# Performance work log

Hardware: AMD Instinct MI355X
Metric: run time of the kernel (lower is better)

Reference implementation:

```python
import jax, jax.numpy as jnp
import numpy as np

DIM = 128
CODEBOOK_SIZE = 1024


def setup_inputs() -> dict:
    key = jax.random.key(0)
    kx, ke = jax.random.split(key)
    x = jax.random.normal(kx, (16, 4096, DIM), dtype=jnp.float32)
    # kaiming_uniform_ on (codebook_size, dim): bound = sqrt(6 / fan_in), fan_in = dim
    bound = float(np.sqrt(6.0 / DIM))
    embed = jax.random.uniform(ke, (CODEBOOK_SIZE, DIM), dtype=jnp.float32,
                               minval=-bound, maxval=bound)
    return {"x": x, "embed": embed}


def reference(x, embed):
    orig_shape = x.shape
    flat = x.reshape(-1, x.shape[-1])                     # [N, D]
    x2 = jnp.sum(flat * flat, axis=1, keepdims=True)      # [N, 1]
    e2 = jnp.sum(embed * embed, axis=1)                   # [K]
    dist = -(x2 - 2.0 * (flat @ embed.T) + e2[None, :])   # [N, K]
    embed_ind = jnp.argmax(dist, axis=-1)                 # [N]
    embed_ind = embed_ind.reshape(orig_shape[:-1])        # [B, S]
    quantize = jnp.take(embed, embed_ind, axis=0)         # [B, S, D]
    return quantize, embed_ind
```

## Files before the change

### kernel.cpp

```cpp
#include <hip/hip_runtime.h>

#define DIM     128
#define NCODES  1024
#define TILE_M  64
#define LDSS    136
#define DELTA   0.02f
#define RPB     4
#define RGRID   1024

typedef __attribute__((ext_vector_type(8))) _Float16 half8;
typedef __attribute__((ext_vector_type(4))) _Float16 half4;
typedef __attribute__((ext_vector_type(4))) float    f32x4;


__global__ __launch_bounds__(256) void setup_kernel(
    const float* __restrict__ embed, double* __restrict__ e2d,
    float* __restrict__ e2f, _Float16* __restrict__ eh,
    float* __restrict__ embedT, int* __restrict__ cnt)
{
  __shared__ float tile[64][132];
  __shared__ double psum[4][64];
  if (blockIdx.x == 0 && threadIdx.x == 0) *cnt = 0;
  const int c0 = blockIdx.x * 64;
  const int t  = threadIdx.x;

  const f32x4* E4 = (const f32x4*)(embed + (size_t)c0 * DIM);
  #pragma unroll
  for (int i = 0; i < 8; ++i) {
    int e = t + i * 256;
    int r = e >> 5, c4 = e & 31;
    f32x4 v = E4[e];
    *(f32x4*)&tile[r][c4 * 4] = v;
    half4 h;
    h[0] = (_Float16)v[0]; h[1] = (_Float16)v[1];
    h[2] = (_Float16)v[2]; h[3] = (_Float16)v[3];
    *(half4*)&eh[(size_t)(c0 + r) * DIM + c4 * 4] = h;
  }
  __syncthreads();

  {
    int r = t & 63, part = t >> 6;
    double s = 0.0;
    #pragma unroll
    for (int k = 0; k < 32; ++k) {
      float v = tile[r][part * 32 + k];
      s += (double)v * v;
    }
    psum[part][r] = s;
  }
  __syncthreads();
  if (t < 64) {
    double s = psum[0][t] + psum[1][t] + psum[2][t] + psum[3][t];
    e2d[c0 + t] = s;
    e2f[c0 + t] = (float)s;
  }

  #pragma unroll
  for (int i = 0; i < 32; ++i) {
    int idx = t + i * 256;
    int k = idx >> 6, c = idx & 63;
    embedT[(size_t)k * NCODES + c0 + c] = tile[c][k];
  }
}

__global__ __launch_bounds__(256)
__attribute__((amdgpu_waves_per_eu(3)))
void pass1_kernel(
    const float* __restrict__ x, const float* __restrict__ embed,
    const _Float16* __restrict__ eh, const float* __restrict__ e2f,
    float* __restrict__ outQ, float* __restrict__ outIdx,
    int* __restrict__ cnt, int* __restrict__ list)
{
  __shared__ _Float16 xh[TILE_M * LDSS];
  __shared__ float rb_best[4][TILE_M];
  __shared__ float rb_sec [4][TILE_M];
  __shared__ int   fidx[TILE_M];

  const int tid  = threadIdx.x;
  const int row0 = blockIdx.x * TILE_M;

  {
    const f32x4* x4 = (const f32x4*)(x + (size_t)row0 * DIM);
    #pragma unroll
    for (int i = 0; i < 8; ++i) {
      int e = tid + i * 256;
      int r = e >> 5, c4 = e & 31;
      f32x4 v = x4[e];
      half4 h;
      h[0] = (_Float16)v[0]; h[1] = (_Float16)v[1];
      h[2] = (_Float16)v[2]; h[3] = (_Float16)v[3];
      *(half4*)&xh[r * LDSS + c4 * 4] = h;
    }
  }
  __syncthreads();

  const int l  = tid & 63, w = tid >> 6;
  const int rl = l & 15,  q = l >> 4;
  const int col0 = q * 8;

  half8 afrag[4][4];
  #pragma unroll
  for (int m = 0; m < 4; ++m)
    #pragma unroll
    for (int ks = 0; ks < 4; ++ks)
      afrag[m][ks] = *(const half8*)&xh[(m * 16 + rl) * LDSS + ks * 32 + col0];

  float bestp[16], secp[16];
  #pragma unroll
  for (int s = 0; s < 16; ++s) { bestp[s] = 3.0e38f; secp[s] = 3.3e38f; }

  const int codeBase = w * 256;
  const _Float16* ehw = eh + (size_t)(codeBase + rl) * DIM + col0;

  half8 bbuf[2][4];
  float e2buf[2];
  #pragma unroll
  for (int ks = 0; ks < 4; ++ks) bbuf[0][ks] = *(const half8*)(ehw + ks * 32);
  e2buf[0] = e2f[codeBase + rl];

  #pragma unroll 2
  for (int ch = 0; ch < 16; ++ch) {
    const int cur = ch & 1, nxt = cur ^ 1;
    const int mycode = codeBase + ch * 16 + rl;
    if (ch < 15) {
      const _Float16* ehn = ehw + (size_t)(ch + 1) * (16 * DIM);
      #pragma unroll
      for (int ks = 0; ks < 4; ++ks) bbuf[nxt][ks] = *(const half8*)(ehn + ks * 32);
      e2buf[nxt] = e2f[mycode + 16];
    }
    const float e2c = e2buf[cur];

    #pragma unroll
    for (int m = 0; m < 4; ++m) {
      f32x4 acc = (f32x4){0.f, 0.f, 0.f, 0.f};
      #pragma unroll
      for (int ks = 0; ks < 4; ++ks)
        acc = __builtin_amdgcn_mfma_f32_16x16x32_f16(afrag[m][ks], bbuf[cur][ks], acc, 0, 0, 0);
      #pragma unroll
      for (int r = 0; r < 4; ++r) {
        const int s = m * 4 + r;
        float sc  = fmaf(-2.0f, acc[r], e2c);
        float scp = __int_as_float((__float_as_int(sc) & ~1023) | mycode);
        secp[s]  = __builtin_amdgcn_fmed3f(bestp[s], scp, secp[s]);
        bestp[s] = fminf(bestp[s], scp);
      }
    }
  }

  #pragma unroll
  for (int off = 1; off < 16; off <<= 1) {
    #pragma unroll
    for (int s = 0; s < 16; ++s) {
      float ob = __shfl_xor(bestp[s], off, 16);
      float os = __shfl_xor(secp[s],  off, 16);
      secp[s]  = fminf(__builtin_amdgcn_fmed3f(bestp[s], ob, secp[s]), os);
      bestp[s] = fminf(bestp[s], ob);
    }
  }
  if (rl == 0) {
    #pragma unroll
    for (int m = 0; m < 4; ++m)
      #pragma unroll
      for (int r = 0; r < 4; ++r) {
        int s = m * 4 + r;
        int row = m * 16 + q * 4 + r;
        rb_best[w][row] = bestp[s];
        rb_sec [w][row] = secp[s];
      }
  }
  __syncthreads();

  if (tid < TILE_M) {
    float bv = rb_best[0][tid], sv = rb_sec[0][tid];
    #pragma unroll
    for (int ww = 1; ww < 4; ++ww) {
      float ob = rb_best[ww][tid], os = rb_sec[ww][tid];
      sv = fminf(__builtin_amdgcn_fmed3f(bv, ob, sv), os);
      bv = fminf(bv, ob);
    }
    int bi = __float_as_int(bv) & 1023;
    int grow = row0 + tid;
    outIdx[grow] = (float)bi;
    fidx[tid] = bi;
    if (sv - bv <= DELTA + fabsf(bv) * 4.8828125e-4f) {
      int p = atomicAdd(cnt, 1);
      list[p] = grow;
    }
  }
  __syncthreads();

  {
    const f32x4* E4   = (const f32x4*)embed;
    f32x4*       out4 = (f32x4*)(outQ + (size_t)row0 * DIM);
    #pragma unroll
    for (int i = 0; i < 8; ++i) {
      int e = tid + i * 256;
      int r = e >> 5, c4 = e & 31;
      out4[e] = E4[fidx[r] * 32 + c4];
    }
  }
}

__global__ __launch_bounds__(256) void refine2_kernel(
    const float* __restrict__ x, const float* __restrict__ embed,
    const float* __restrict__ embedT,
    const double* __restrict__ e2d, const float* __restrict__ e2f,
    float* __restrict__ outQ, float* __restrict__ outIdx,
    const int* __restrict__ cnt, const int* __restrict__ list)
{
  __shared__ f32x4 xst[DIM];
  __shared__ float rb1[RPB][4], rb2[RPB][4];
  __shared__ int   ri1[RPB][4], ri2[RPB][4];
  __shared__ int   cand[RPB][2];

  const int t = threadIdx.x;
  const int l = t & 63, w = t >> 6;
  const int n = *cnt;
  float* xsf = (float*)xst;

  for (int base = blockIdx.x * RPB; base < n; base += RGRID * RPB) {
    const int nr = min(RPB, n - base);
    #pragma unroll
    for (int i = 0; i < 2; ++i) {
      int idx = t + i * 256;
      int r = idx >> 7, k = idx & 127;
      float v = 0.f;
      if (r < nr) v = x[(size_t)list[base + r] * DIM + k];
      xsf[k * RPB + r] = v;
    }
    __syncthreads();

    f32x4 dot[RPB];
    #pragma unroll
    for (int r = 0; r < RPB; ++r) dot[r] = (f32x4){0.f, 0.f, 0.f, 0.f};
    const f32x4* eT4 = (const f32x4*)embedT;
    #pragma unroll 4
    for (int k = 0; k < DIM; ++k) {
      f32x4 e4  = eT4[k * 256 + t];
      f32x4 xk4 = xst[k];
      #pragma unroll
      for (int r = 0; r < RPB; ++r) {
        dot[r][0] = fmaf(xk4[r], e4[0], dot[r][0]);
        dot[r][1] = fmaf(xk4[r], e4[1], dot[r][1]);
        dot[r][2] = fmaf(xk4[r], e4[2], dot[r][2]);
        dot[r][3] = fmaf(xk4[r], e4[3], dot[r][3]);
      }
    }

    #pragma unroll
    for (int r = 0; r < RPB; ++r) {
      float b1 = 3.4e38f, b2 = 3.4e38f; int i1 = 0, i2 = 0;
      #pragma unroll
      for (int j = 0; j < 4; ++j) {
        int c = 4 * t + j;
        float sc = fmaf(-2.0f, dot[r][j], e2f[c]);
        bool better = (sc < b1);
        float lv = better ? b1 : sc;  int li = better ? i1 : c;
        if (better) { b1 = sc; i1 = c; }
        bool t2 = (lv < b2) || (lv == b2 && li < i2);
        if (t2) { b2 = lv; i2 = li; }
      }
      #pragma unroll
      for (int off = 1; off < 64; off <<= 1) {
        float o1 = __shfl_xor(b1, off, 64); int oi1 = __shfl_xor(i1, off, 64);
        float o2 = __shfl_xor(b2, off, 64); int oi2 = __shfl_xor(i2, off, 64);
        bool take = (o1 < b1) || (o1 == b1 && oi1 < i1);
        float n1 = take ? o1 : b1; int ni1 = take ? oi1 : i1;
        float lo = take ? b1 : o1; int loi = take ? i1 : oi1;
        float c2v = take ? o2 : b2; int c2i = take ? oi2 : i2;
        bool u2 = (c2v < lo) || (c2v == lo && c2i < loi);
        b1 = n1; i1 = ni1;
        b2 = u2 ? c2v : lo; i2 = u2 ? c2i : loi;
      }
      if (l == 0) { rb1[r][w] = b1; ri1[r][w] = i1; rb2[r][w] = b2; ri2[r][w] = i2; }
    }
    __syncthreads();

    if (t < RPB) {
      float v1 = rb1[t][0], v2 = rb2[t][0]; int j1 = ri1[t][0], j2 = ri2[t][0];
      #pragma unroll
      for (int ww = 1; ww < 4; ++ww) {
        float o1 = rb1[t][ww], o2 = rb2[t][ww]; int oi1 = ri1[t][ww], oi2 = ri2[t][ww];
        bool take = (o1 < v1) || (o1 == v1 && oi1 < j1);
        float n1 = take ? o1 : v1; int ni1 = take ? oi1 : j1;
        float lo = take ? v1 : o1; int loi = take ? j1 : oi1;
        float c2v = take ? o2 : v2; int c2i = take ? oi2 : j2;
        bool u2 = (c2v < lo) || (c2v == lo && c2i < loi);
        v1 = n1; j1 = ni1; v2 = u2 ? c2v : lo; j2 = u2 ? c2i : loi;
      }
      cand[t][0] = j1; cand[t][1] = j2;
    }
    __syncthreads();

    if (w < nr) {
      int c1 = cand[w][0], c2 = cand[w][1];
      float xa = xsf[l * RPB + w], xb = xsf[(l + 64) * RPB + w];
      double p1 = (double)xa * (double)embed[(size_t)c1 * DIM + l]
                + (double)xb * (double)embed[(size_t)c1 * DIM + 64 + l];
      double p2 = (double)xa * (double)embed[(size_t)c2 * DIM + l]
                + (double)xb * (double)embed[(size_t)c2 * DIM + 64 + l];
      #pragma unroll
      for (int off = 1; off < 64; off <<= 1) {
        p1 += __shfl_xor(p1, off, 64);
        p2 += __shfl_xor(p2, off, 64);
      }
      double s1 = e2d[c1] - 2.0 * p1;
      double s2 = e2d[c2] - 2.0 * p2;
      int widx = ((s2 < s1) || (s2 == s1 && c2 < c1)) ? c2 : c1;
      int row = list[base + w];
      if (l == 0) outIdx[row] = (float)widx;
      outQ[(size_t)row * DIM + l]      = embed[(size_t)widx * DIM + l];
      outQ[(size_t)row * DIM + 64 + l] = embed[(size_t)widx * DIM + 64 + l];
    }
    __syncthreads();
  }
}

extern "C" void kernel_launch(void* const* d_in, const int* in_sizes, int n_in,
                              void* d_out, int out_size, void* d_ws, size_t ws_size,
                              hipStream_t stream) {
  const float* x     = (const float*)d_in[0];
  const float* embed = (const float*)d_in[1];
  const int N = in_sizes[0] / DIM;

  float* out    = (float*)d_out;
  float* outQ   = out;
  float* outIdx = out + (size_t)N * DIM;

  char* ws = (char*)d_ws;
  double*   e2d  = (double*)  (ws);
  float*    e2f  = (float*)   (ws + 8192);
  _Float16* eh   = (_Float16*)(ws + 12288);
  float*    eT   = (float*)   (ws + 274432);
  int*      cnt  = (int*)     (ws + 798720);
  int*      list = (int*)     (ws + 798976);

  setup_kernel  <<<NCODES / 64, 256, 0, stream>>>(embed, e2d, e2f, eh, eT, cnt);
  pass1_kernel  <<<N / TILE_M,  256, 0, stream>>>(x, embed, eh, e2f, outQ, outIdx, cnt, list);
  refine2_kernel<<<RGRID,       256, 0, stream>>>(x, embed, eT, e2d, e2f, outQ, outIdx, cnt, list);
}
```

Before: 145.5 us.

## Split pass1 tile across 8 waves and fold norm into MFMA accumulator init

The pass1 kernel now runs 512 threads per block, with 8 waves each covering 32 rows by 256 codes instead of 64 rows. This halves the A fragments and best/second registers per thread, which should raise occupancy. The score becomes a maximised quantity: the accumulator is seeded with -0.5*e2 minus a constant, which removes the per-element fma after the MFMA. The ambiguity check becomes a fixed absolute margin with no relative term, which could change how many rows get flagged for refinement and risks missing close ties at large magnitudes.

```diff
diff --git a/kernel.cpp b/kernel.cpp
--- a/kernel.cpp
+++ b/kernel.cpp
@@ -4,7 +4,7 @@
 #define NCODES  1024
 #define TILE_M  64
 #define LDSS    136
-#define DELTA   0.02f
+#define FLAGThr 0.018f
 #define RPB     4
 #define RGRID   1024
 
@@ -63,8 +63,8 @@
   }
 }
 
-__global__ __launch_bounds__(256)
-__attribute__((amdgpu_waves_per_eu(3)))
+__global__ __launch_bounds__(512)
+__attribute__((amdgpu_waves_per_eu(4)))
 void pass1_kernel(
     const float* __restrict__ x, const float* __restrict__ embed,
     const _Float16* __restrict__ eh, const float* __restrict__ e2f,
@@ -82,8 +82,8 @@
   {
     const f32x4* x4 = (const f32x4*)(x + (size_t)row0 * DIM);
     #pragma unroll
-    for (int i = 0; i < 8; ++i) {
-      int e = tid + i * 256;
+    for (int i = 0; i < 4; ++i) {
+      int e = tid + i * 512;
       int r = e >> 5, c4 = e & 31;
       f32x4 v = x4[e];
       half4 h;
@@ -97,19 +97,21 @@
   const int l  = tid & 63, w = tid >> 6;
   const int rl = l & 15,  q = l >> 4;
   const int col0 = q * 8;
-
-  half8 afrag[4][4];
-  #pragma unroll
-  for (int m = 0; m < 4; ++m)
+  const int rh = w >> 2;
+  const int cq = w & 3;
+
+  half8 afrag[2][4];
+  #pragma unroll
+  for (int m = 0; m < 2; ++m)
     #pragma unroll
     for (int ks = 0; ks < 4; ++ks)
-      afrag[m][ks] = *(const half8*)&xh[(m * 16 + rl) * LDSS + ks * 32 + col0];
-
-  float bestp[16], secp[16];
-  #pragma unroll
-  for (int s = 0; s < 16; ++s) { bestp[s] = 3.0e38f; secp[s] = 3.3e38f; }
-
-  const int codeBase = w * 256;
+      afrag[m][ks] = *(const half8*)&xh[(rh * 32 + m * 16 + rl) * LDSS + ks * 32 + col0];
+
+  float bestp[8], secp[8];
+  #pragma unroll
+  for (int s = 0; s < 8; ++s) { bestp[s] = -3.0e38f; secp[s] = -3.3e38f; }
+
+  const int codeBase = cq * 256;
   const _Float16* ehw = eh + (size_t)(codeBase + rl) * DIM + col0;
 
   half8 bbuf[2][4];
@@ -128,21 +130,20 @@
       for (int ks = 0; ks < 4; ++ks) bbuf[nxt][ks] = *(const half8*)(ehn + ks * 32);
       e2buf[nxt] = e2f[mycode + 16];
     }
-    const float e2c = e2buf[cur];
-
-    #pragma unroll
-    for (int m = 0; m < 4; ++m) {
-      f32x4 acc = (f32x4){0.f, 0.f, 0.f, 0.f};
+    const float vinit = fmaf(-0.5f, e2buf[cur], -16.0f);
+
+    #pragma unroll
+    for (int m = 0; m < 2; ++m) {
+      f32x4 acc = (f32x4){vinit, vinit, vinit, vinit};
       #pragma unroll
       for (int ks = 0; ks < 4; ++ks)
         acc = __builtin_amdgcn_mfma_f32_16x16x32_f16(afrag[m][ks], bbuf[cur][ks], acc, 0, 0, 0);
       #pragma unroll
       for (int r = 0; r < 4; ++r) {
         const int s = m * 4 + r;
-        float sc  = fmaf(-2.0f, acc[r], e2c);
-        float scp = __int_as_float((__float_as_int(sc) & ~1023) | mycode);
-        secp[s]  = __builtin_amdgcn_fmed3f(bestp[s], scp, secp[s]);
-        bestp[s] = fminf(bestp[s], scp);
+        float scp = __int_as_float((__float_as_int(acc[r]) & ~1023) | mycode);
+        secp[s]  = __builtin_amdgcn_fmed3f(scp, bestp[s], secp[s]);
+        bestp[s] = fmaxf(bestp[s], scp);
       }
     }
   }
@@ -150,22 +151,22 @@
   #pragma unroll
   for (int off = 1; off < 16; off <<= 1) {
     #pragma unroll
-    for (int s = 0; s < 16; ++s) {
+    for (int s = 0; s < 8; ++s) {
       float ob = __shfl_xor(bestp[s], off, 16);
       float os = __shfl_xor(secp[s],  off, 16);
-      secp[s]  = fminf(__builtin_amdgcn_fmed3f(bestp[s], ob, secp[s]), os);
-      bestp[s] = fminf(bestp[s], ob);
+      secp[s]  = fmaxf(__builtin_amdgcn_fmed3f(bestp[s], ob, secp[s]), os);
+      bestp[s] = fmaxf(bestp[s], ob);
     }
   }
   if (rl == 0) {
     #pragma unroll
-    for (int m = 0; m < 4; ++m)
+    for (int m = 0; m < 2; ++m)
       #pragma unroll
       for (int r = 0; r < 4; ++r) {
         int s = m * 4 + r;
-        int row = m * 16 + q * 4 + r;
-        rb_best[w][row] = bestp[s];
-        rb_sec [w][row] = secp[s];
+        int row = rh * 32 + m * 16 + q * 4 + r;
+        rb_best[cq][row] = bestp[s];
+        rb_sec [cq][row] = secp[s];
       }
   }
   __syncthreads();
@@ -173,16 +174,16 @@
   if (tid < TILE_M) {
     float bv = rb_best[0][tid], sv = rb_sec[0][tid];
     #pragma unroll
-    for (int ww = 1; ww < 4; ++ww) {
-      float ob = rb_best[ww][tid], os = rb_sec[ww][tid];
-      sv = fminf(__builtin_amdgcn_fmed3f(bv, ob, sv), os);
-      bv = fminf(bv, ob);
+    for (int c2 = 1; c2 < 4; ++c2) {
+      float ob = rb_best[c2][tid], os = rb_sec[c2][tid];
+      sv = fmaxf(__builtin_amdgcn_fmed3f(bv, ob, sv), os);
+      bv = fmaxf(bv, ob);
     }
     int bi = __float_as_int(bv) & 1023;
     int grow = row0 + tid;
     outIdx[grow] = (float)bi;
     fidx[tid] = bi;
-    if (sv - bv <= DELTA + fabsf(bv) * 4.8828125e-4f) {
+    if (bv - sv <= FLAGThr) {
       int p = atomicAdd(cnt, 1);
       list[p] = grow;
     }
@@ -193,8 +194,8 @@
     const f32x4* E4   = (const f32x4*)embed;
     f32x4*       out4 = (f32x4*)(outQ + (size_t)row0 * DIM);
     #pragma unroll
-    for (int i = 0; i < 8; ++i) {
-      int e = tid + i * 256;
+    for (int i = 0; i < 4; ++i) {
+      int e = tid + i * 512;
       int r = e >> 5, c4 = e & 31;
       out4[e] = E4[fidx[r] * 32 + c4];
     }
@@ -336,6 +337,6 @@
   int*      list = (int*)     (ws + 798976);
 
   setup_kernel  <<<NCODES / 64, 256, 0, stream>>>(embed, e2d, e2f, eh, eT, cnt);
-  pass1_kernel  <<<N / TILE_M,  256, 0, stream>>>(x, embed, eh, e2f, outQ, outIdx, cnt, list);
+  pass1_kernel  <<<N / TILE_M,  512, 0, stream>>>(x, embed, eh, e2f, outQ, outIdx, cnt, list);
   refine2_kernel<<<RGRID,       256, 0, stream>>>(x, embed, eT, e2d, e2f, outQ, outIdx, cnt, list);
 }
```

Measured after the change: 165.4 us. 1.14x slower.

## Stage fp16 codebook chunks in LDS and fold e2 bias into MFMA accumulator init

Applied to the files above, without the earlier changes.

Replaces the per-wave direct global reads of the fp16 codebook with a block-cooperative load of 256-code chunks into padded LDS, software-pipelined through registers across four stages. The score is flipped to a maximization of x·e - 0.5||e||^2 - 16, with the bias preloaded into the MFMA accumulator so the per-element fma disappears. The constant offset keeps the scores negative, which the index-packing trick in the float bits relies on. The MFMA loop is reordered so each B fragment feeds four independent accumulators, and the tie-flag threshold is replaced by a fixed absolute margin. In exchange the kernel uses much more LDS and adds block-wide barriers per stage; launch bounds change to request 2 blocks.

```diff
diff --git a/kernel.cpp b/kernel.cpp
--- a/kernel.cpp
+++ b/kernel.cpp
@@ -3,8 +3,8 @@
 #define DIM     128
 #define NCODES  1024
 #define TILE_M  64
-#define LDSS    136
-#define DELTA   0.02f
+#define BSTR    272
+#define FLAGThr 0.018f
 #define RPB     4
 #define RGRID   1024
 
@@ -63,21 +63,20 @@
   }
 }
 
-__global__ __launch_bounds__(256)
-__attribute__((amdgpu_waves_per_eu(3)))
-void pass1_kernel(
+__global__ __launch_bounds__(256, 2) void pass1_kernel(
     const float* __restrict__ x, const float* __restrict__ embed,
     const _Float16* __restrict__ eh, const float* __restrict__ e2f,
     float* __restrict__ outQ, float* __restrict__ outIdx,
     int* __restrict__ cnt, int* __restrict__ list)
 {
-  __shared__ _Float16 xh[TILE_M * LDSS];
+  __shared__ __align__(16) unsigned char lds[256 * BSTR];
   __shared__ float rb_best[4][TILE_M];
   __shared__ float rb_sec [4][TILE_M];
   __shared__ int   fidx[TILE_M];
 
   const int tid  = threadIdx.x;
   const int row0 = blockIdx.x * TILE_M;
+  _Float16* xh = (_Float16*)lds;
 
   {
     const f32x4* x4 = (const f32x4*)(x + (size_t)row0 * DIM);
@@ -89,7 +88,7 @@
       half4 h;
       h[0] = (_Float16)v[0]; h[1] = (_Float16)v[1];
       h[2] = (_Float16)v[2]; h[3] = (_Float16)v[3];
-      *(half4*)&xh[r * LDSS + c4 * 4] = h;
+      *(half4*)&xh[r * 136 + c4 * 4] = h;
     }
   }
   __syncthreads();
@@ -103,47 +102,71 @@
   for (int m = 0; m < 4; ++m)
     #pragma unroll
     for (int ks = 0; ks < 4; ++ks)
-      afrag[m][ks] = *(const half8*)&xh[(m * 16 + rl) * LDSS + ks * 32 + col0];
+      afrag[m][ks] = *(const half8*)&xh[(m * 16 + rl) * 136 + ks * 32 + col0];
 
   float bestp[16], secp[16];
   #pragma unroll
-  for (int s = 0; s < 16; ++s) { bestp[s] = 3.0e38f; secp[s] = 3.3e38f; }
-
-  const int codeBase = w * 256;
-  const _Float16* ehw = eh + (size_t)(codeBase + rl) * DIM + col0;
-
-  half8 bbuf[2][4];
-  float e2buf[2];
-  #pragma unroll
-  for (int ks = 0; ks < 4; ++ks) bbuf[0][ks] = *(const half8*)(ehw + ks * 32);
-  e2buf[0] = e2f[codeBase + rl];
-
-  #pragma unroll 2
-  for (int ch = 0; ch < 16; ++ch) {
-    const int cur = ch & 1, nxt = cur ^ 1;
-    const int mycode = codeBase + ch * 16 + rl;
-    if (ch < 15) {
-      const _Float16* ehn = ehw + (size_t)(ch + 1) * (16 * DIM);
-      #pragma unroll
-      for (int ks = 0; ks < 4; ++ks) bbuf[nxt][ks] = *(const half8*)(ehn + ks * 32);
-      e2buf[nxt] = e2f[mycode + 16];
-    }
-    const float e2c = e2buf[cur];
-
-    #pragma unroll
-    for (int m = 0; m < 4; ++m) {
-      f32x4 acc = (f32x4){0.f, 0.f, 0.f, 0.f};
+  for (int s = 0; s < 16; ++s) { bestp[s] = -3.0e38f; secp[s] = -3.3e38f; }
+
+  f32x4 t0[16];
+  {
+    const f32x4* src = (const f32x4*)eh;
+    #pragma unroll
+    for (int i = 0; i < 16; ++i) t0[i] = src[tid + i * 256];
+  }
+  __syncthreads();
+
+  #pragma unroll
+  for (int st = 0; st < 4; ++st) {
+    #pragma unroll
+    for (int i = 0; i < 16; ++i) {
+      int e = tid + i * 256;
+      *(f32x4*)&lds[(e >> 4) * BSTR + (e & 15) * 16] = t0[i];
+    }
+    f32x4 t1[16];
+    if (st < 3) {
+      const f32x4* src = (const f32x4*)(eh + (size_t)(st + 1) * 256 * DIM);
+      #pragma unroll
+      for (int i = 0; i < 16; ++i) t1[i] = src[tid + i * 256];
+    }
+    float vinit[4];
+    #pragma unroll
+    for (int sub = 0; sub < 4; ++sub)
+      vinit[sub] = fmaf(-0.5f, e2f[st * 256 + w * 64 + sub * 16 + rl], -16.0f);
+
+    __syncthreads();
+
+    #pragma unroll
+    for (int sub = 0; sub < 4; ++sub) {
+      const int codeL  = w * 64 + sub * 16 + rl;
+      const int mycode = st * 256 + codeL;
+      half8 bfrag[4];
       #pragma unroll
       for (int ks = 0; ks < 4; ++ks)
-        acc = __builtin_amdgcn_mfma_f32_16x16x32_f16(afrag[m][ks], bbuf[cur][ks], acc, 0, 0, 0);
-      #pragma unroll
-      for (int r = 0; r < 4; ++r) {
-        const int s = m * 4 + r;
-        float sc  = fmaf(-2.0f, acc[r], e2c);
-        float scp = __int_as_float((__float_as_int(sc) & ~1023) | mycode);
-        secp[s]  = __builtin_amdgcn_fmed3f(bestp[s], scp, secp[s]);
-        bestp[s] = fminf(bestp[s], scp);
-      }
+        bfrag[ks] = *(const half8*)&lds[codeL * BSTR + ks * 64 + q * 16];
+      f32x4 acc[4];
+      #pragma unroll
+      for (int m = 0; m < 4; ++m)
+        acc[m] = (f32x4){vinit[sub], vinit[sub], vinit[sub], vinit[sub]};
+      #pragma unroll
+      for (int ks = 0; ks < 4; ++ks)
+        #pragma unroll
+        for (int m = 0; m < 4; ++m)
+          acc[m] = __builtin_amdgcn_mfma_f32_16x16x32_f16(afrag[m][ks], bfrag[ks], acc[m], 0, 0, 0);
+      #pragma unroll
+      for (int m = 0; m < 4; ++m)
+        #pragma unroll
+        for (int r = 0; r < 4; ++r) {
+          const int s = m * 4 + r;
+          float scp = __int_as_float((__float_as_int(acc[m][r]) & ~1023) | mycode);
+          secp[s]  = __builtin_amdgcn_fmed3f(scp, bestp[s], secp[s]);
+          bestp[s] = fmaxf(bestp[s], scp);
+        }
+    }
+    if (st < 3) {
+      __syncthreads();
+      #pragma unroll
+      for (int i = 0; i < 16; ++i) t0[i] = t1[i];
     }
   }
 
@@ -153,8 +176,8 @@
     for (int s = 0; s < 16; ++s) {
       float ob = __shfl_xor(bestp[s], off, 16);
       float os = __shfl_xor(secp[s],  off, 16);
-      secp[s]  = fminf(__builtin_amdgcn_fmed3f(bestp[s], ob, secp[s]), os);
-      bestp[s] = fminf(bestp[s], ob);
+      secp[s]  = fmaxf(__builtin_amdgcn_fmed3f(bestp[s], ob, secp[s]), os);
+      bestp[s] = fmaxf(bestp[s], ob);
     }
   }
   if (rl == 0) {
@@ -175,14 +198,14 @@
     #pragma unroll
     for (int ww = 1; ww < 4; ++ww) {
       float ob = rb_best[ww][tid], os = rb_sec[ww][tid];
-      sv = fminf(__builtin_amdgcn_fmed3f(bv, ob, sv), os);
-      bv = fminf(bv, ob);
+      sv = fmaxf(__builtin_amdgcn_fmed3f(bv, ob, sv), os);
+      bv = fmaxf(bv, ob);
     }
     int bi = __float_as_int(bv) & 1023;
     int grow = row0 + tid;
     outIdx[grow] = (float)bi;
     fidx[tid] = bi;
-    if (sv - bv <= DELTA + fabsf(bv) * 4.8828125e-4f) {
+    if (bv - sv <= FLAGThr) {
       int p = atomicAdd(cnt, 1);
       list[p] = grow;
     }
```

Measured after the change: 140.6 us. -3.4%, faster.
